# Performance work log

Hardware: AMD Instinct MI355X
Metric: run time of the kernel (lower is better)

## Reference

```python
import jax, jax.numpy as jnp
import numpy as np
from jax import lax


def _conv(x, w, b, pad, dil):
    # standard NCHW conv, OIHW weights
    y = lax.conv_general_dilated(x, w, (1, 1), [(pad, pad), (pad, pad)],
                                 rhs_dilation=(dil, dil),
                                 dimension_numbers=('NCHW', 'OIHW', 'NCHW'))
    return y + b[None, :, None, None]


def _bilinear(img, py, px):
    # img: [B,C,H,W]; py,px: [B,KK,H,W] float sample positions.
    # Zero-padding bilinear sampling (torchvision deform_conv semantics):
    # each of the 4 corners contributes 0 if it lies outside the image.
    B, C, H, W = img.shape
    y0 = jnp.floor(py)
    x0 = jnp.floor(px)
    wy1 = py - y0
    wx1 = px - x0
    imgf = img.reshape(B, C, H * W)

    def corner(yi, xi, wgt):
        valid = (yi >= 0) & (yi <= H - 1) & (xi >= 0) & (xi <= W - 1)
        yc = jnp.clip(yi, 0, H - 1).astype(jnp.int32)
        xc = jnp.clip(xi, 0, W - 1).astype(jnp.int32)
        idx = yc * W + xc  # [B,KK,H,W]
        g = jax.vmap(lambda im, ix: jnp.take(im, ix.reshape(-1), axis=1))(imgf, idx)
        g = g.reshape(B, C, *yi.shape[1:])  # [B,C,KK,H,W]
        return g * (wgt * valid.astype(img.dtype))[:, None]

    return (corner(y0, x0, (1 - wy1) * (1 - wx1))
            + corner(y0, x0 + 1, (1 - wy1) * wx1)
            + corner(y0 + 1, x0, wy1 * (1 - wx1))
            + corner(y0 + 1, x0 + 1, wy1 * wx1))


def _deform_dw(x, off_w, off_b, dw_w, K, pad, dil):
    # offset-predicted deformable depthwise conv (groups == channels)
    B, C, H, W = x.shape
    off = _conv(x, off_w, off_b, pad, dil).reshape(B, K * K, 2, H, W)
    dy, dx = off[:, :, 0], off[:, :, 1]  # torchvision order: (dy, dx) per tap
    ky, kx = jnp.meshgrid(jnp.arange(K), jnp.arange(K), indexing='ij')
    by = (ky.reshape(-1) * dil - pad).astype(x.dtype)  # [KK]
    bx = (kx.reshape(-1) * dil - pad).astype(x.dtype)
    py = jnp.arange(H, dtype=x.dtype)[None, None, :, None] + by[None, :, None, None] + dy
    px = jnp.arange(W, dtype=x.dtype)[None, None, None, :] + bx[None, :, None, None] + dx
    s = _bilinear(x, py, px)  # [B,C,KK,H,W]
    return jnp.einsum('bckhw,ck->bchw', s, dw_w.reshape(C, K * K))


def setup_inputs() -> dict:
    key = jax.random.key(0)
    ks = jax.random.split(key, 9)
    B, C, H, W = 4, 64, 56, 56
    f = lambda k, shape, s: jax.random.normal(k, shape, jnp.float32) * s
    return dict(
        x=f(ks[0], (B, C, H, W), 1.0),
        off_w1=f(ks[1], (2 * 5 * 5, C, 5, 5), 0.01), off_b1=f(ks[2], (2 * 5 * 5,), 0.01),
        dw_w1=f(ks[3], (C, 1, 5, 5), 0.1),
        off_w2=f(ks[4], (2 * 7 * 7, C, 7, 7), 0.01), off_b2=f(ks[5], (2 * 7 * 7,), 0.01),
        dw_w2=f(ks[6], (C, 1, 7, 7), 0.1),
        pw_w=f(ks[7], (C, C, 1, 1), 0.05), pw_b=f(ks[8], (C,), 0.05),
    )


def reference(x, off_w1, off_b1, dw_w1, off_w2, off_b2, dw_w2, pw_w, pw_b):
    attn = _deform_dw(x, off_w1, off_b1, dw_w1, 5, 2, 1)       # 5x5 deformable dw
    attn = _deform_dw(attn, off_w2, off_b2, dw_w2, 7, 9, 3)    # 7x7 dil-3 deformable dw
    attn = _conv(attn, pw_w, pw_b, 0, 1)                       # 1x1 pointwise
    return x * attn                                            # gated multiply
```

## Files before the change

### kernel.cpp

```cpp
#include <hip/hip_runtime.h>

#define BB 4
#define CC 64
#define HH 56
#define WW 56
#define HW (HH*WW)

typedef unsigned short u16;
typedef __attribute__((ext_vector_type(8))) short bf16x8;
typedef __attribute__((ext_vector_type(4))) float f32x4;

__device__ __forceinline__ u16 f2bf(float f) {
    union { float f; unsigned u; } c; c.f = f;
    unsigned u = c.u;
    u = (u + 0x7FFFu + ((u >> 16) & 1u)) >> 16;
    return (u16)u;
}
__device__ __forceinline__ float bf2f(u16 v) {
    union { unsigned u; float f; } c; c.u = ((unsigned)v) << 16;
    return c.f;
}

#define R1 102400
#define R2 401408
#define R3 4096
#define R4 1600
#define R5 3136
__global__ __launch_bounds__(256)
void prep_all_kernel(const float* __restrict__ ow1, const float* __restrict__ ow2,
                     const float* __restrict__ pw,  const float* __restrict__ dw1,
                     const float* __restrict__ dw2,
                     u16* __restrict__ w2t1, u16* __restrict__ w2t2,
                     u16* __restrict__ pwT, float* __restrict__ dwT1,
                     float* __restrict__ dwT2) {
    const int i = blockIdx.x*256 + threadIdx.x;
    if (i < R1) {
        const int ic = i & 63, n = (i >> 6) & 63, tap = i >> 12;
        w2t1[i] = f2bf((n < 50) ? ow1[((size_t)n*64 + ic)*25 + tap] : 0.f);
    } else if (i < R1+R2) {
        const int j = i - R1;
        const int ic = j & 63, n = (j >> 6) & 127, tap = j >> 13;
        w2t2[j] = f2bf((n < 98) ? ow2[((size_t)n*64 + ic)*49 + tap] : 0.f);
    } else if (i < R1+R2+R3) {
        const int j = i - (R1+R2);
        pwT[j] = f2bf(pw[j]);
    } else if (i < R1+R2+R3+R4) {
        const int j = i - (R1+R2+R3);
        const int c = j & 63, k = j >> 6;
        dwT1[j] = dw1[c*25 + k];
    } else if (i < R1+R2+R3+R4+R5) {
        const int j = i - (R1+R2+R3+R4);
        const int c = j & 63, k = j >> 6;
        dwT2[j] = dw2[c*49 + k];
    }
}

__global__ __launch_bounds__(256)
void transpose_bf16_kernel(const float* __restrict__ in, u16* __restrict__ out) {
    __shared__ u16 tile[64][72];
    const int blk = blockIdx.x;
    const int b   = blk / (HW/64);
    const int p0  = (blk % (HW/64))*64;
    const int t   = threadIdx.x;

    const int px  = t & 63, icq = t >> 6;
    const float* ip = in + ((size_t)b*CC + icq*16)*HW + p0 + px;
    #pragma unroll
    for (int i = 0; i < 16; ++i)
        tile[px][icq*16 + i] = f2bf(ip[(size_t)i*HW]);
    __syncthreads();

    const int px2 = t >> 2, g = t & 3;
    u16* op = out + ((size_t)b*HW + p0 + px2)*64 + g*16;
    const uint4* s = (const uint4*)&tile[px2][g*16];
    ((uint4*)op)[0] = s[0];
    ((uint4*)op)[1] = s[1];
}

__device__ __forceinline__ uint4 selz(bool v, uint4 a) {
    const uint4 z = make_uint4(0,0,0,0);
    return v ? a : z;
}

template<int K, int DIL, int PAD, int COUT, int NP, int NPAD, int NTW>
__global__ __launch_bounds__(256, 4)
void conv_mfma_lds_kernel(const u16* __restrict__ xT, const u16* __restrict__ w2t,
                          const float* __restrict__ bias, float* __restrict__ out) {
    constexpr int KK = K*K;
    constexpr int BROWS = 16*NTW;
    __shared__ u16 Ab[2][64*64];
    __shared__ u16 Bb[2][BROWS*64];

    const int nm   = HW/64;
    const int b    = blockIdx.x / nm;
    const int p0   = (blockIdx.x % nm)*64;
    const int nt0  = blockIdx.y;
    const int t    = threadIdx.x;
    const int wave = t >> 6;
    const int lane = t & 63;

    const int spx = t >> 3;
    const int sc  = t & 7;
    const int pA  = p0 + spx;
    const int pB  = p0 + spx + 32;
    const int pyA = pA / WW, pxA = pA % WW;
    const int pyB = pB / WW, pxB = pB % WW;
    const u16* xb = xT + (size_t)b*HW*64;
    const int sslotA = ((sc + spx) & 7)*8;
    const int bn  = t >> 3;
    const int bslot = ((sc + bn) & 7)*8;
    const u16* wbase = w2t + (size_t)nt0*BROWS*64;

    const int r = lane & 15, quad = lane >> 4;
    const int mloc = wave*16 + r;
    const int arow = mloc*64;
    const int a0s = ((quad     + mloc) & 7)*8;
    const int a1s = ((quad + 4 + mloc) & 7)*8;
    const int b0s = ((quad     + r) & 7)*8;
    const int b1s = ((quad + 4 + r) & 7)*8;

    f32x4 acc[NTW];
    #pragma unroll
    for (int h = 0; h < NTW; ++h) acc[h] = (f32x4){0.f,0.f,0.f,0.f};
    const uint4 z4 = make_uint4(0,0,0,0);

    auto LD = [&](int tap, uint4& a0, uint4& a1, bool& va, bool& vb, uint4& bb) {
        const int dyy = (tap/K)*DIL - PAD;
        const int dxx = (tap%K)*DIL - PAD;
        const int off = dyy*WW + dxx;
        {
            const int yy = pyA + dyy, xx = pxA + dxx;
            va = ((unsigned)yy < (unsigned)HH) && ((unsigned)xx < (unsigned)WW);
            a0 = *(const uint4*)(xb + (size_t)(va ? (pA + off) : 0)*64 + sc*8);
        }
        {
            const int yy = pyB + dyy, xx = pxB + dxx;
            vb = ((unsigned)yy < (unsigned)HH) && ((unsigned)xx < (unsigned)WW);
            a1 = *(const uint4*)(xb + (size_t)(vb ? (pB + off) : 0)*64 + sc*8);
        }
        if (BROWS == 32 || bn < BROWS)
            bb = *(const uint4*)(wbase + ((size_t)tap*NP + bn)*64 + sc*8);
    };

    uint4 rA0 = z4, rA1 = z4, rB = z4;
    bool v0 = false, v1 = false;
    LD(0, rA0, rA1, v0, v1, rB);

    #pragma unroll
    for (int tap = 0; tap < KK; ++tap) {
        uint4 nA0 = z4, nA1 = z4, nB = z4;
        bool nv0 = false, nv1 = false;
        if (tap + 1 < KK) LD(tap + 1, nA0, nA1, nv0, nv1, nB);

        u16* A  = &Ab[tap & 1][0];
        u16* Bq = &Bb[tap & 1][0];
        *(uint4*)(A + spx*64      + sslotA) = selz(v0, rA0);
        *(uint4*)(A + (spx+32)*64 + sslotA) = selz(v1, rA1);
        if (BROWS == 32 || bn < BROWS) *(uint4*)(Bq + bn*64 + bslot) = rB;
        __syncthreads();

        const bf16x8 av0 = *(const bf16x8*)(A + arow + a0s);
        const bf16x8 av1 = *(const bf16x8*)(A + arow + a1s);
        #pragma unroll
        for (int h = 0; h < NTW; ++h) {
            const int brow = (h*16 + r)*64;
            const bf16x8 bv0 = *(const bf16x8*)(Bq + brow + b0s);
            const bf16x8 bv1 = *(const bf16x8*)(Bq + brow + b1s);
            acc[h] = __builtin_amdgcn_mfma_f32_16x16x32_bf16(av0, bv0, acc[h], 0, 0, 0);
            acc[h] = __builtin_amdgcn_mfma_f32_16x16x32_bf16(av1, bv1, acc[h], 0, 0, 0);
        }

        rA0 = nA0; rA1 = nA1; rB = nB; v0 = nv0; v1 = nv1;
    }

    #pragma unroll
    for (int h = 0; h < NTW; ++h) {
        const int n = nt0*BROWS + h*16 + r;
        if (n < COUT) {
            const float bv = bias[n];
            float* op = out + ((size_t)b*HW + p0 + wave*16 + quad*4)*NPAD + n;
            #pragma unroll
            for (int r2 = 0; r2 < 4; ++r2) op[(size_t)r2*NPAD] = acc[h][r2] + bv;
        }
    }
}

template<int K, int DIL, int PAD, int NPAD>
__global__ __launch_bounds__(256)
void deform_cl_kernel(const u16* __restrict__ inT, const float* __restrict__ offT,
                      const float* __restrict__ dwT, u16* __restrict__ outT) {
    constexpr int KK = K*K;
    __shared__ float4 swt[4][KK];
    __shared__ int4   sat[4][KK];
    __shared__ float  sdw[KK*64];

    const int t = threadIdx.x;
    const int nb8 = (BB*HW/4) >> 3;
    const int blk0 = blockIdx.x;
    const int blk = (blk0 & 7)*nb8 + (blk0 >> 3);
    const int p0 = blk*4;
    const int b  = p0 / HW;
    const int pl0 = p0 - b*HW;

    for (int i = t; i < KK*64; i += 256) sdw[i] = dwT[i];

    if (t < 4*KK) {
        const int pix = t / KK, k = t - pix*KK;
        const int pl  = pl0 + pix;
        const int h = pl / WW, w = pl % WW;
        const float* orow = offT + ((size_t)b*HW + pl)*NPAD;
        const float dy = orow[2*k];
        const float dx = orow[2*k+1];
        const float py = (float)(h + (k/K)*DIL - PAD) + dy;
        const float px = (float)(w + (k%K)*DIL - PAD) + dx;
        const float y0f = floorf(py), x0f = floorf(px);
        const float wy1 = py - y0f,  wx1 = px - x0f;
        const float wy0 = 1.f - wy1, wx0 = 1.f - wx1;
        const int y0 = (int)y0f, x0 = (int)x0f;

        const int y0c = min(max(y0,   0), HH-1);
        const int y1c = min(max(y0+1, 0), HH-1);
        const int x0c = min(max(x0,   0), WW-1);
        const int x1c = min(max(x0+1, 0), WW-1);
        const float gy0 = wy0 * ((y0   >= 0 && y0   < HH) ? 1.f : 0.f);
        const float gy1 = wy1 * ((y0+1 >= 0 && y0+1 < HH) ? 1.f : 0.f);
        const float gx0 = wx0 * ((x0   >= 0 && x0   < WW) ? 1.f : 0.f);
        const float gx1 = wx1 * ((x0+1 >= 0 && x0+1 < WW) ? 1.f : 0.f);

        swt[pix][k] = make_float4(gy0*gx0, gy0*gx1, gy1*gx0, gy1*gx1);
        const int r0 = y0c*WW, r1 = y1c*WW;
        sat[pix][k] = make_int4((r0 + x0c) << 7, (r0 + x1c) << 7,
                                (r1 + x0c) << 7, (r1 + x1c) << 7);
    }
    __syncthreads();

    const int wave = t >> 6, lane = t & 63;
    const char* ib = (const char*)(inT + (size_t)b*HW*64) + lane*2;

    float acc = 0.f;
    #pragma unroll 7
    for (int k = 0; k < KK; ++k) {
        const float4 wv = swt[wave][k];
        const int4   av = sat[wave][k];
        const float v00 = bf2f(*(const u16*)(ib + av.x));
        const float v01 = bf2f(*(const u16*)(ib + av.y));
        const float v10 = bf2f(*(const u16*)(ib + av.z));
        const float v11 = bf2f(*(const u16*)(ib + av.w));
        const float s = v00*wv.x + v01*wv.y + v10*wv.z + v11*wv.w;
        acc += s * sdw[k*64 + lane];
    }
    outT[(size_t)(p0 + wave)*64 + lane] = f2bf(acc);
}

__global__ __launch_bounds__(256)
void pw_mfma_kernel(const u16* __restrict__ a2T, const u16* __restrict__ pwT,
                    const float* __restrict__ pb, const float* __restrict__ x,
                    float* __restrict__ out) {
    const int nm = HW/64;
    const int b  = blockIdx.x / nm;
    const int p0 = (blockIdx.x % nm)*64 + (threadIdx.x >> 6)*16;
    const int nt = blockIdx.y;
    const int lane = threadIdx.x & 63;
    const int r = lane & 15, quad = lane >> 4;

    const u16* ap = a2T + ((size_t)b*HW + p0 + r)*64 + quad*8;
    f32x4 acc = (f32x4){0.f,0.f,0.f,0.f};
    #pragma unroll
    for (int ks = 0; ks < 2; ++ks) {
        const bf16x8 av = *(const bf16x8*)(ap + ks*32);
        const bf16x8 bv = *(const bf16x8*)(pwT + ((size_t)(nt*16 + r))*64 + ks*32 + quad*8);
        acc = __builtin_amdgcn_mfma_f32_16x16x32_bf16(av, bv, acc, 0, 0, 0);
    }

    const int n = nt*16 + r;
    const float bv = pb[n];
    const size_t base = ((size_t)b*CC + n)*HW + p0 + quad*4;
    #pragma unroll
    for (int r2 = 0; r2 < 4; ++r2)
        out[base + r2] = x[base + r2] * (acc[r2] + bv);
}

template<int K, int DIL, int PAD, int COUT, int OCB>
__global__ __launch_bounds__(256)
void off_conv_sg_kernel(const float* __restrict__ in, const float* __restrict__ wgt,
                        const float* __restrict__ bias, float* __restrict__ out) {
    constexpr int KK = K*K;
    const int nOB = COUT / OCB;
    const int b   = blockIdx.x / nOB;
    const int oc0 = (blockIdx.x % nOB) * OCB;
    const int x   = threadIdx.x;
    const int h   = blockIdx.y*4 + threadIdx.y;

    float acc[OCB];
    #pragma unroll
    for (int o = 0; o < OCB; ++o) acc[o] = bias[oc0+o];

    const float* inb = in + (size_t)b*CC*HW;
    const float* wb  = wgt + (size_t)oc0*CC*KK;

    for (int ic = 0; ic < CC; ++ic) {
        const float* inp = inb + ic*HW;
        const float* wp  = wb + ic*KK;
        #pragma unroll
        for (int ky = 0; ky < K; ++ky) {
            const int  y  = h + ky*DIL - PAD;
            const bool yv = (y >= 0) && (y < HH);
            const int  yc = yv ? y : 0;
            const float* row = inp + yc*WW;
            #pragma unroll
            for (int kx = 0; kx < K; ++kx) {
                const int  xx = x + kx*DIL - PAD;
                const bool v  = yv && (xx >= 0) && (xx < WW);
                const int  xc = (xx < 0) ? 0 : ((xx >= WW) ? (WW-1) : xx);
                float val = row[xc];
                val = v ? val : 0.f;
                const int t = ky*K + kx;
                #pragma unroll
                for (int o = 0; o < OCB; ++o)
                    acc[o] += wp[(size_t)o*CC*KK + t] * val;
            }
        }
    }

    if (x >= WW) return;
    #pragma unroll
    for (int o = 0; o < OCB; ++o)
        out[((size_t)b*COUT + oc0 + o)*HW + h*WW + x] = acc[o];
}

template<int K, int DIL, int PAD>
__global__ __launch_bounds__(64)
void deform_dw_full_kernel(const float* __restrict__ in, const float* __restrict__ off,
                           const float* __restrict__ dw, float* __restrict__ out) {
    constexpr int KK = K*K;
    const int idx = blockIdx.x*64 + threadIdx.x;
    const int x = idx % WW;
    const int h = (idx / WW) % HH;
    const int c = (idx / HW) % CC;
    const int b = idx / (CC*HW);

    const float* inp  = in  + ((size_t)b*CC + c)*HW;
    const float* offp = off + (size_t)b*(2*KK)*HW + h*WW + x;
    const float* dwp  = dw  + c*KK;

    float acc = 0.f;
    #pragma unroll 7
    for (int k = 0; k < KK; ++k) {
        const float dy = offp[(2*k  )*HW];
        const float dx = offp[(2*k+1)*HW];
        const float py = (float)(h + (k/K)*DIL - PAD) + dy;
        const float px = (float)(x + (k%K)*DIL - PAD) + dx;
        const float y0f = floorf(py), x0f = floorf(px);
        const float wy1 = py - y0f,  wx1 = px - x0f;
        const float wy0 = 1.f - wy1, wx0 = 1.f - wx1;
        const int y0 = (int)y0f, x0 = (int)x0f;

        const int y0c = min(max(y0,   0), HH-1);
        const int y1c = min(max(y0+1, 0), HH-1);
        const int x0c = min(max(x0,   0), WW-1);
        const int x1c = min(max(x0+1, 0), WW-1);
        const float my0 = (y0   >= 0 && y0   < HH) ? 1.f : 0.f;
        const float my1 = (y0+1 >= 0 && y0+1 < HH) ? 1.f : 0.f;
        const float mx0 = (x0   >= 0 && x0   < WW) ? 1.f : 0.f;
        const float mx1 = (x0+1 >= 0 && x0+1 < WW) ? 1.f : 0.f;

        const float v00 = inp[y0c*WW + x0c];
        const float v01 = inp[y0c*WW + x1c];
        const float v10 = inp[y1c*WW + x0c];
        const float v11 = inp[y1c*WW + x1c];

        const float gx0 = wx0*mx0, gx1 = wx1*mx1;
        const float s = (v00*gx0 + v01*gx1) * (wy0*my0)
                      + (v10*gx0 + v11*gx1) * (wy1*my1);
        acc += s * dwp[k];
    }
    out[idx] = acc;
}

__global__ __launch_bounds__(256)
void pw_mul_kernel(const float* __restrict__ x, const float* __restrict__ a2,
                   const float* __restrict__ pw, const float* __restrict__ pb,
                   float* __restrict__ out) {
    constexpr int HW4 = HW/4;
    const int t = blockIdx.x*256 + threadIdx.x;
    if (t >= BB*CC*HW4) return;
    const int sp4 = t % HW4;
    const int oc  = (t / HW4) % CC;
    const int b   = t / (CC*HW4);

    const float4* ap = (const float4*)(a2 + (size_t)b*CC*HW) + sp4;
    const float4* wp4 = (const float4*)(pw + oc*CC);
    const float pbv = pb[oc];
    float4 acc = make_float4(pbv, pbv, pbv, pbv);
    #pragma unroll 4
    for (int ic4 = 0; ic4 < CC/4; ++ic4) {
        const float4 w = wp4[ic4];
        float4 a0 = ap[(ic4*4+0)*HW4];
        float4 a1 = ap[(ic4*4+1)*HW4];
        float4 a2v = ap[(ic4*4+2)*HW4];
        float4 a3 = ap[(ic4*4+3)*HW4];
        acc.x += w.x*a0.x + w.y*a1.x + w.z*a2v.x + w.w*a3.x;
        acc.y += w.x*a0.y + w.y*a1.y + w.z*a2v.y + w.w*a3.y;
        acc.z += w.x*a0.z + w.y*a1.z + w.z*a2v.z + w.w*a3.z;
        acc.w += w.x*a0.w + w.y*a1.w + w.z*a2v.w + w.w*a3.w;
    }
    const float4 xv = ((const float4*)x)[t];
    float4 r;
    r.x = xv.x*acc.x; r.y = xv.y*acc.y; r.z = xv.z*acc.z; r.w = xv.w*acc.w;
    ((float4*)out)[t] = r;
}

extern "C" void kernel_launch(void* const* d_in, const int* in_sizes, int n_in,
                              void* d_out, int out_size, void* d_ws, size_t ws_size,
                              hipStream_t stream) {
    const float* x      = (const float*)d_in[0];
    const float* off_w1 = (const float*)d_in[1];
    const float* off_b1 = (const float*)d_in[2];
    const float* dw_w1  = (const float*)d_in[3];
    const float* off_w2 = (const float*)d_in[4];
    const float* off_b2 = (const float*)d_in[5];
    const float* dw_w2  = (const float*)d_in[6];
    const float* pw_w   = (const float*)d_in[7];
    const float* pw_b   = (const float*)d_in[8];
    float* out = (float*)d_out;

    const size_t nF    = (size_t)BB*CC*HW;
    const size_t attnB = nF*sizeof(float);
    const size_t off2B = (size_t)BB*98*HW*sizeof(float);
    const size_t offTB = (size_t)BB*HW*112*sizeof(float);
    const size_t chB   = (size_t)BB*HW*64*sizeof(u16);
    char* ws = (char*)d_ws;

    const int n    = (int)nF;
    const int dbl  = n/64;
    const int pbl  = (n/4 + 255)/256;
    dim3 cblk(64,4);
    dim3 rgrd1(BB*(50/5), HH/4);
    dim3 rgrd2(BB*(98/7), HH/4);
    const int tgrid = BB*(HW/64);
    dim3 cgrd1(tgrid, 2);
    dim3 cgrd2(tgrid, 4);
    dim3 pgrd(tgrid, 4);
    const int dgrid = BB*HW/4;

    const size_t oOFF  = 0;
    const size_t oXT   = oOFF + offTB;
    const size_t oA1T  = oXT  + chB;
    const size_t oA2T  = oA1T + chB;
    const size_t oW1   = oA2T + chB;
    const size_t oW2   = oW1  + (size_t)R1*2;
    const size_t oPWT  = oW2  + (size_t)R2*2;
    const size_t oDW1  = oPWT + (size_t)R3*2;
    const size_t oDW2  = oDW1 + (size_t)R4*4;
    const size_t TOT   = oDW2 + (size_t)R5*4;

    if (ws_size >= TOT) {
        float* off_buf = (float*)(ws + oOFF);
        u16*   xT      = (u16*)(ws + oXT);
        u16*   a1T     = (u16*)(ws + oA1T);
        u16*   a2T     = (u16*)(ws + oA2T);
        u16*   w2t1    = (u16*)(ws + oW1);
        u16*   w2t2    = (u16*)(ws + oW2);
        u16*   pwT     = (u16*)(ws + oPWT);
        float* dwT1    = (float*)(ws + oDW1);
        float* dwT2    = (float*)(ws + oDW2);

        prep_all_kernel<<<(R1+R2+R3+R4+R5+255)/256, 256, 0, stream>>>(
            off_w1, off_w2, pw_w, dw_w1, dw_w2, w2t1, w2t2, pwT, dwT1, dwT2);
        transpose_bf16_kernel<<<tgrid, 256, 0, stream>>>(x, xT);

        conv_mfma_lds_kernel<5,1,2,50,64,64,2><<<cgrd1, 256, 0, stream>>>(xT, w2t1, off_b1, off_buf);
        deform_cl_kernel<5,1,2,64><<<dgrid, 256, 0, stream>>>(xT, off_buf, dwT1, a1T);

        conv_mfma_lds_kernel<7,3,9,98,128,112,2><<<cgrd2, 256, 0, stream>>>(a1T, w2t2, off_b2, off_buf);
        deform_cl_kernel<7,3,9,112><<<dgrid, 256, 0, stream>>>(a1T, off_buf, dwT2, a2T);

        pw_mfma_kernel<<<pgrd, 256, 0, stream>>>(a2T, pwT, pw_b, x, out);
    } else if (ws_size >= off2B + attnB) {
        float* off_buf = (float*)ws;
        float* attn1   = (float*)d_out;
        float* attn2   = (float*)(ws + off2B);
        off_conv_sg_kernel<5,1,2,50,5><<<rgrd1, cblk, 0, stream>>>(x, off_w1, off_b1, off_buf);
        deform_dw_full_kernel<5,1,2><<<dbl, 64, 0, stream>>>(x, off_buf, dw_w1, attn1);
        off_conv_sg_kernel<7,3,9,98,7><<<rgrd2, cblk, 0, stream>>>(attn1, off_w2, off_b2, off_buf);
        deform_dw_full_kernel<7,3,9><<<dbl, 64, 0, stream>>>(attn1, off_buf, dw_w2, attn2);
        pw_mul_kernel<<<pbl, 256, 0, stream>>>(x, attn2, pw_w, pw_b, out);
    } else {
        float* attn1 = (float*)d_out;
        float* attn2 = (float*)ws;
        float* off1  = (float*)ws;
        off_conv_sg_kernel<5,1,2,50,5><<<rgrd1, cblk, 0, stream>>>(x, off_w1, off_b1, off1);
        deform_dw_full_kernel<5,1,2><<<dbl, 64, 0, stream>>>(x, off1, dw_w1, attn1);
        float* off2 = (float*)(ws + attnB);
        off_conv_sg_kernel<7,3,9,98,7><<<rgrd2, cblk, 0, stream>>>(attn1, off_w2, off_b2, off2);
        deform_dw_full_kernel<7,3,9><<<dbl, 64, 0, stream>>>(attn1, off2, dw_w2, attn2);
        pw_mul_kernel<<<pbl, 256, 0, stream>>>(x, attn2, pw_w, pw_b, out);
    }
}
```

Baseline: 175.9 us.

## Merge input transpose into weight prep kernel; process 8 pixels per deform block

Folds the NCHW-to-channels-last bf16 transpose into the weight-preparation kernel, so one launch does both jobs and a kernel boundary goes away. The deformable sampling kernel now handles 8 pixels per block. Each lane reads two bf16 channels with a single 32-bit load and keeps two accumulators, which halves the gather instruction count per output and the per-pixel launch overhead. The offset-precompute stage loops to cover 8*KK entries, so the grid shrinks and per-thread work goes up.

```diff
diff --git a/kernel.cpp b/kernel.cpp
--- a/kernel.cpp
+++ b/kernel.cpp
@@ -7,6 +7,7 @@
 #define HW (HH*WW)
 
 typedef unsigned short u16;
+typedef unsigned int u32;
 typedef __attribute__((ext_vector_type(8))) short bf16x8;
 typedef __attribute__((ext_vector_type(4))) float f32x4;
 
@@ -20,20 +21,49 @@
     union { unsigned u; float f; } c; c.u = ((unsigned)v) << 16;
     return c.f;
 }
+__device__ __forceinline__ float lo_f(u32 u) {
+    union { unsigned u; float f; } c; c.u = u << 16; return c.f;
+}
+__device__ __forceinline__ float hi_f(u32 u) {
+    union { unsigned u; float f; } c; c.u = u & 0xffff0000u; return c.f;
+}
 
 #define R1 102400
 #define R2 401408
 #define R3 4096
 #define R4 1600
 #define R5 3136
+#define TGRID (BB*(HW/64))
+#define PREPN (R1+R2+R3+R4+R5)
 __global__ __launch_bounds__(256)
-void prep_all_kernel(const float* __restrict__ ow1, const float* __restrict__ ow2,
-                     const float* __restrict__ pw,  const float* __restrict__ dw1,
-                     const float* __restrict__ dw2,
-                     u16* __restrict__ w2t1, u16* __restrict__ w2t2,
-                     u16* __restrict__ pwT, float* __restrict__ dwT1,
-                     float* __restrict__ dwT2) {
-    const int i = blockIdx.x*256 + threadIdx.x;
+void prep_tr_kernel(const float* __restrict__ x,
+                    const float* __restrict__ ow1, const float* __restrict__ ow2,
+                    const float* __restrict__ pw,  const float* __restrict__ dw1,
+                    const float* __restrict__ dw2,
+                    u16* __restrict__ xT,
+                    u16* __restrict__ w2t1, u16* __restrict__ w2t2,
+                    u16* __restrict__ pwT, float* __restrict__ dwT1,
+                    float* __restrict__ dwT2) {
+    __shared__ u16 tile[64][72];
+    const int t = threadIdx.x;
+    if (blockIdx.x < TGRID) {
+        const int blk = blockIdx.x;
+        const int b   = blk / (HW/64);
+        const int p0  = (blk % (HW/64))*64;
+        const int px  = t & 63, icq = t >> 6;
+        const float* ip = x + ((size_t)b*CC + icq*16)*HW + p0 + px;
+        #pragma unroll
+        for (int i = 0; i < 16; ++i)
+            tile[px][icq*16 + i] = f2bf(ip[(size_t)i*HW]);
+        __syncthreads();
+        const int px2 = t >> 2, g = t & 3;
+        u16* op = xT + ((size_t)b*HW + p0 + px2)*64 + g*16;
+        const uint4* s = (const uint4*)&tile[px2][g*16];
+        ((uint4*)op)[0] = s[0];
+        ((uint4*)op)[1] = s[1];
+        return;
+    }
+    const int i = (blockIdx.x - TGRID)*256 + t;
     if (i < R1) {
         const int ic = i & 63, n = (i >> 6) & 63, tap = i >> 12;
         w2t1[i] = f2bf((n < 50) ? ow1[((size_t)n*64 + ic)*25 + tap] : 0.f);
@@ -55,28 +85,6 @@
     }
 }
 
-__global__ __launch_bounds__(256)
-void transpose_bf16_kernel(const float* __restrict__ in, u16* __restrict__ out) {
-    __shared__ u16 tile[64][72];
-    const int blk = blockIdx.x;
-    const int b   = blk / (HW/64);
-    const int p0  = (blk % (HW/64))*64;
-    const int t   = threadIdx.x;
-
-    const int px  = t & 63, icq = t >> 6;
-    const float* ip = in + ((size_t)b*CC + icq*16)*HW + p0 + px;
-    #pragma unroll
-    for (int i = 0; i < 16; ++i)
-        tile[px][icq*16 + i] = f2bf(ip[(size_t)i*HW]);
-    __syncthreads();
-
-    const int px2 = t >> 2, g = t & 3;
-    u16* op = out + ((size_t)b*HW + p0 + px2)*64 + g*16;
-    const uint4* s = (const uint4*)&tile[px2][g*16];
-    ((uint4*)op)[0] = s[0];
-    ((uint4*)op)[1] = s[1];
-}
-
 __device__ __forceinline__ uint4 selz(bool v, uint4 a) {
     const uint4 z = make_uint4(0,0,0,0);
     return v ? a : z;
@@ -190,22 +198,22 @@
 void deform_cl_kernel(const u16* __restrict__ inT, const float* __restrict__ offT,
                       const float* __restrict__ dwT, u16* __restrict__ outT) {
     constexpr int KK = K*K;
-    __shared__ float4 swt[4][KK];
-    __shared__ int4   sat[4][KK];
+    __shared__ float4 swt[8][KK];
+    __shared__ int4   sat[8][KK];
     __shared__ float  sdw[KK*64];
 
     const int t = threadIdx.x;
-    const int nb8 = (BB*HW/4) >> 3;
+    const int nb8 = (BB*HW/8) >> 3;
     const int blk0 = blockIdx.x;
     const int blk = (blk0 & 7)*nb8 + (blk0 >> 3);
-    const int p0 = blk*4;
+    const int p0 = blk*8;
     const int b  = p0 / HW;
     const int pl0 = p0 - b*HW;
 
     for (int i = t; i < KK*64; i += 256) sdw[i] = dwT[i];
 
-    if (t < 4*KK) {
-        const int pix = t / KK, k = t - pix*KK;
+    for (int i = t; i < 8*KK; i += 256) {
+        const int pix = i / KK, k = i - pix*KK;
         const int pl  = pl0 + pix;
         const int h = pl / WW, w = pl % WW;
         const float* orow = offT + ((size_t)b*HW + pl)*NPAD;
@@ -235,21 +243,27 @@
     __syncthreads();
 
     const int wave = t >> 6, lane = t & 63;
-    const char* ib = (const char*)(inT + (size_t)b*HW*64) + lane*2;
-
-    float acc = 0.f;
+    const int pixl = 2*wave + (lane >> 5);
+    const int chp  = lane & 31;
+    const char* ib = (const char*)(inT + (size_t)b*HW*64) + chp*4;
+
+    float accx = 0.f, accy = 0.f;
     #pragma unroll 7
     for (int k = 0; k < KK; ++k) {
-        const float4 wv = swt[wave][k];
-        const int4   av = sat[wave][k];
-        const float v00 = bf2f(*(const u16*)(ib + av.x));
-        const float v01 = bf2f(*(const u16*)(ib + av.y));
-        const float v10 = bf2f(*(const u16*)(ib + av.z));
-        const float v11 = bf2f(*(const u16*)(ib + av.w));
-        const float s = v00*wv.x + v01*wv.y + v10*wv.z + v11*wv.w;
-        acc += s * sdw[k*64 + lane];
-    }
-    outT[(size_t)(p0 + wave)*64 + lane] = f2bf(acc);
+        const float4 wv = swt[pixl][k];
+        const int4   av = sat[pixl][k];
+        const u32 c00 = *(const u32*)(ib + av.x);
+        const u32 c01 = *(const u32*)(ib + av.y);
+        const u32 c10 = *(const u32*)(ib + av.z);
+        const u32 c11 = *(const u32*)(ib + av.w);
+        const float sx = lo_f(c00)*wv.x + lo_f(c01)*wv.y + lo_f(c10)*wv.z + lo_f(c11)*wv.w;
+        const float sy = hi_f(c00)*wv.x + hi_f(c01)*wv.y + hi_f(c10)*wv.z + hi_f(c11)*wv.w;
+        const float2 dw2 = *(const float2*)&sdw[k*64 + 2*chp];
+        accx += sx * dw2.x;
+        accy += sy * dw2.y;
+    }
+    const u32 o = (u32)f2bf(accx) | ((u32)f2bf(accy) << 16);
+    *(u32*)((char*)outT + (size_t)(p0 + pixl)*128 + chp*4) = o;
 }
 
 __global__ __launch_bounds__(256)
@@ -437,11 +451,10 @@
     dim3 cblk(64,4);
     dim3 rgrd1(BB*(50/5), HH/4);
     dim3 rgrd2(BB*(98/7), HH/4);
-    const int tgrid = BB*(HW/64);
-    dim3 cgrd1(tgrid, 2);
-    dim3 cgrd2(tgrid, 4);
-    dim3 pgrd(tgrid, 4);
-    const int dgrid = BB*HW/4;
+    dim3 cgrd1(TGRID, 2);
+    dim3 cgrd2(TGRID, 4);
+    dim3 pgrd(TGRID, 4);
+    const int dgrid = BB*HW/8;
 
     const size_t oOFF  = 0;
     const size_t oXT   = oOFF + offTB;
@@ -465,9 +478,9 @@
         float* dwT1    = (float*)(ws + oDW1);
         float* dwT2    = (float*)(ws + oDW2);
 
-        prep_all_kernel<<<(R1+R2+R3+R4+R5+255)/256, 256, 0, stream>>>(
-            off_w1, off_w2, pw_w, dw_w1, dw_w2, w2t1, w2t2, pwT, dwT1, dwT2);
-        transpose_bf16_kernel<<<tgrid, 256, 0, stream>>>(x, xT);
+        prep_tr_kernel<<<TGRID + (PREPN+255)/256, 256, 0, stream>>>(
+            x, off_w1, off_w2, pw_w, dw_w1, dw_w2,
+            xT, w2t1, w2t2, pwT, dwT1, dwT2);
 
         conv_mfma_lds_kernel<5,1,2,50,64,64,2><<<cgrd1, 256, 0, stream>>>(xT, w2t1, off_b1, off_buf);
         deform_cl_kernel<5,1,2,64><<<dgrid, 256, 0, stream>>>(xT, off_buf, dwT1, a1T);
```

New measurement: 158.9 us. -9.6%, faster.
